# Optimization experiments

Measured on AMD Instinct MI355X. Metric: run time of the kernel, lower is better.

## Reference

```python
import jax, jax.numpy as jnp
import numpy as np

N_PRED = 29
F_DIM = 8192
H1 = 256
H2 = 128


def setup_inputs() -> dict:
    key = jax.random.key(0)
    ks = jax.random.split(key, 7)
    features = jax.random.normal(ks[0], (4096, F_DIM), dtype=jnp.float32)
    # Stacked per-predicate MLP weights (PyTorch Linear init scale ~ 1/sqrt(fan_in))
    W1 = jax.random.normal(ks[1], (N_PRED, F_DIM, H1), dtype=jnp.float32) / np.sqrt(F_DIM)
    b1 = jax.random.normal(ks[2], (N_PRED, H1), dtype=jnp.float32) / np.sqrt(F_DIM)
    W2 = jax.random.normal(ks[3], (N_PRED, H1, H2), dtype=jnp.float32) / np.sqrt(H1)
    b2 = jax.random.normal(ks[4], (N_PRED, H2), dtype=jnp.float32) / np.sqrt(H1)
    W3 = jax.random.normal(ks[5], (N_PRED, H2), dtype=jnp.float32) / np.sqrt(H2)
    b3 = jax.random.normal(ks[6], (N_PRED,), dtype=jnp.float32) / np.sqrt(H2)
    return {"features": features, "W1": W1, "b1": b1, "W2": W2, "b2": b2, "W3": W3, "b3": b3}


def reference(features, W1, b1, W2, b2, W3, b3):
    # 29 parallel heads as one batched (grouped) GEMM chain; dropout = identity (eval).
    h1 = jax.nn.relu(jnp.einsum('bf,pfh->bph', features, W1) + b1[None])   # [B, P, H1]
    h2 = jax.nn.relu(jnp.einsum('bph,phk->bpk', h1, W2) + b2[None])        # [B, P, H2]
    logits = jnp.einsum('bpk,pk->bp', h2, W3) + b3[None]                   # [B, P]
    return jax.nn.sigmoid(logits)
```

## Files before the change

### kernel.cpp

```cpp
#include <hip/hip_runtime.h>
#include <hip/hip_bf16.h>

typedef __attribute__((ext_vector_type(8))) short short8_t;
typedef __attribute__((ext_vector_type(8))) __bf16 bf16x8;
typedef __attribute__((ext_vector_type(4))) float f32x4;

__device__ __forceinline__ void gload16(const void* g, void* l) {
  __builtin_amdgcn_global_load_lds(
      (const __attribute__((address_space(1))) void*)g,
      (__attribute__((address_space(3))) void*)l, 16, 0, 0);
}

__device__ __forceinline__ unsigned short f2bf(float f) {
  __hip_bfloat16 h = __float2bfloat16(f);
  return __builtin_bit_cast(unsigned short, h);
}

#define BARRIER() asm volatile("s_barrier" ::: "memory")


__global__ void k_cvt_feat(const float* __restrict__ in, unsigned short* __restrict__ out) {
  const size_t N = (size_t)4096 * 8192;
  size_t i = ((size_t)blockIdx.x * 256 + threadIdx.x) * 4;
  const size_t stride = (size_t)gridDim.x * 256 * 4;
  for (; i < N; i += stride) {
    float4 v = *(const float4*)(in + i);
    ushort4 o;
    o.x = f2bf(v.x); o.y = f2bf(v.y); o.z = f2bf(v.z); o.w = f2bf(v.w);
    *(ushort4*)(out + i) = o;
  }
}

__global__ void k_cvt_w1(const float* __restrict__ W1, unsigned short* __restrict__ out, int p0) {
  __shared__ unsigned short t[64][262];
  const int p = p0 + blockIdx.z;
  const float* src = W1 + (size_t)p * 8192 * 256;
  unsigned short* dst = out + (size_t)blockIdx.z * 256 * 8192;
  const int f0 = blockIdx.x * 256, h0 = blockIdx.y * 64;
#pragma unroll
  for (int i = 0; i < 64; ++i) {
    int tt = i * 256 + threadIdx.x;
    int f = tt >> 6, c = tt & 63;
    t[c][f] = f2bf(src[(size_t)(f0 + f) * 256 + h0 + c]);
  }
  __syncthreads();
#pragma unroll
  for (int i = 0; i < 8; ++i) {
    int tt = i * 256 + threadIdx.x;
    int r = tt >> 5;
    int c8 = (tt & 31) * 8;
    short8_t o;
#pragma unroll
    for (int j = 0; j < 8; ++j) o[j] = (short)t[r][c8 + j];
    *(short8_t*)&dst[(size_t)(h0 + r) * 8192 + f0 + c8] = o;
  }
}

__global__ void k_cvt_w2(const float* __restrict__ W2, unsigned short* __restrict__ out) {
  const int p = blockIdx.x;
  const float* src = W2 + (size_t)p * 256 * 128;
  unsigned short* dst = out + (size_t)p * 128 * 256;
  for (int tt = threadIdx.x; tt < 128 * 256; tt += 256) {
    int j = tt >> 8, h = tt & 255;
    dst[tt] = f2bf(src[(size_t)h * 128 + j]);
  }
}

__global__ __launch_bounds__(512, 2) void k_gemm1(
    const unsigned short* __restrict__ A,
    const unsigned short* __restrict__ Bt,
    const float* __restrict__ b1,
    const unsigned short* __restrict__ W2t,
    const float* __restrict__ b2,
    const float* __restrict__ W3,
    const float* __restrict__ b3,
    float* __restrict__ out,
    int p0) {
  __shared__ __align__(16) unsigned short S[65536];

  const int tid = threadIdx.x;
  const int lane = tid & 63;
  const int wave = tid >> 6;
  const int sr = (wave >> 2) * 64;
  const int sc = (wave & 3) * 32;

  const int nwg = gridDim.x * gridDim.y;
  const int orig = blockIdx.y * gridDim.x + blockIdx.x;
  const int q = nwg >> 3, r_ = nwg & 7;
  const int xcd = orig & 7, idx = orig >> 3;
  const int wg = (xcd < r_ ? xcd * (q + 1) : r_ * (q + 1) + (xcd - r_) * q) + idx;
  const int mx = wg & 15;
  const int z = wg >> 4;
  const int p = p0 + z;
  const int m0 = mx * 256;

  const unsigned short* Ab = A + (size_t)m0 * 8192;
  const unsigned short* Bb = Bt + (size_t)z * 256 * 8192;

  int e0 = tid, r0 = e0 >> 3, u0 = (e0 & 7) ^ (r0 & 7);
  int e1 = 512 + tid, r1e = e1 >> 3, u1 = (e1 & 7) ^ (r1e & 7);
  const size_t s0 = (size_t)r0 * 8192 + u0 * 8;
  const size_t s1 = (size_t)r1e * 8192 + u1 * 8;
  const int ld0 = (wave * 64) * 8;
  const int ld1 = (512 + wave * 64) * 8;

  auto stage = [&](int buf, int isB, int h, int T) {
    const unsigned short* gb = (isB ? Bb : Ab) + (size_t)h * 128 * 8192 + (size_t)T * 64;
    unsigned short* lb = S + buf * 32768 + isB * 16384 + h * 8192;
    gload16(gb + s0, lb + ld0);
    gload16(gb + s1, lb + ld1);
  };

  const int l15 = lane & 15, ks = lane >> 4;

  auto rdA = [&](int buf, int h, int mi, int x) {
    int R = sr + mi * 16 + l15;
    int pu = (x * 4 + ks) ^ (R & 7);
    return __builtin_bit_cast(bf16x8, *(const short8_t*)(S + buf * 32768 + h * 8192 + R * 64 + pu * 8));
  };
  auto rdB = [&](int buf, int v, int nj, int x) {
    int R = sc + nj * 16 + l15;
    int pu = (x * 4 + ks) ^ (R & 7);
    return __builtin_bit_cast(bf16x8, *(const short8_t*)(S + buf * 32768 + 16384 + v * 8192 + R * 64 + pu * 8));
  };

  f32x4 acc[4][4][2] = {};
  const int NT = 8192 / 64;

  auto kstep = [&](int t, int pfa, int pf, int vm) {
    const int c = t & 1, nx = c ^ 1;
    bf16x8 a[4][2], bl[2][2], bh[2][2];
#pragma unroll
    for (int mi = 0; mi < 4; ++mi) { a[mi][0] = rdA(c, 0, mi, 0); a[mi][1] = rdA(c, 0, mi, 1); }
#pragma unroll
    for (int nj = 0; nj < 2; ++nj) { bl[nj][0] = rdB(c, 0, nj, 0); bl[nj][1] = rdB(c, 0, nj, 1); }
    if (pfa) stage(nx, 0, 1, t + 1);
    BARRIER();
    __builtin_amdgcn_s_setprio(1);
#pragma unroll
    for (int mi = 0; mi < 4; ++mi)
#pragma unroll
      for (int nj = 0; nj < 2; ++nj) {
        acc[0][mi][nj] = __builtin_amdgcn_mfma_f32_16x16x32_bf16(a[mi][0], bl[nj][0], acc[0][mi][nj], 0, 0, 0);
        acc[0][mi][nj] = __builtin_amdgcn_mfma_f32_16x16x32_bf16(a[mi][1], bl[nj][1], acc[0][mi][nj], 0, 0, 0);
      }
    __builtin_amdgcn_s_setprio(0);
    BARRIER();
#pragma unroll
    for (int nj = 0; nj < 2; ++nj) { bh[nj][0] = rdB(c, 1, nj, 0); bh[nj][1] = rdB(c, 1, nj, 1); }
    if (pf) stage(c, 0, 0, t + 2);
    BARRIER();
    __builtin_amdgcn_s_setprio(1);
#pragma unroll
    for (int mi = 0; mi < 4; ++mi)
#pragma unroll
      for (int nj = 0; nj < 2; ++nj) {
        acc[1][mi][nj] = __builtin_amdgcn_mfma_f32_16x16x32_bf16(a[mi][0], bh[nj][0], acc[1][mi][nj], 0, 0, 0);
        acc[1][mi][nj] = __builtin_amdgcn_mfma_f32_16x16x32_bf16(a[mi][1], bh[nj][1], acc[1][mi][nj], 0, 0, 0);
      }
    __builtin_amdgcn_s_setprio(0);
    BARRIER();
#pragma unroll
    for (int mi = 0; mi < 4; ++mi) { a[mi][0] = rdA(c, 1, mi, 0); a[mi][1] = rdA(c, 1, mi, 1); }
    if (pf) stage(c, 1, 1, t + 2);
    BARRIER();
    __builtin_amdgcn_s_setprio(1);
#pragma unroll
    for (int mi = 0; mi < 4; ++mi)
#pragma unroll
      for (int nj = 0; nj < 2; ++nj) {
        acc[2][mi][nj] = __builtin_amdgcn_mfma_f32_16x16x32_bf16(a[mi][0], bl[nj][0], acc[2][mi][nj], 0, 0, 0);
        acc[2][mi][nj] = __builtin_amdgcn_mfma_f32_16x16x32_bf16(a[mi][1], bl[nj][1], acc[2][mi][nj], 0, 0, 0);
      }
    __builtin_amdgcn_s_setprio(0);
    BARRIER();
    if (pf) stage(c, 1, 0, t + 2);
    __builtin_amdgcn_s_setprio(1);
#pragma unroll
    for (int mi = 0; mi < 4; ++mi)
#pragma unroll
      for (int nj = 0; nj < 2; ++nj) {
        acc[3][mi][nj] = __builtin_amdgcn_mfma_f32_16x16x32_bf16(a[mi][0], bh[nj][0], acc[3][mi][nj], 0, 0, 0);
        acc[3][mi][nj] = __builtin_amdgcn_mfma_f32_16x16x32_bf16(a[mi][1], bh[nj][1], acc[3][mi][nj], 0, 0, 0);
      }
    __builtin_amdgcn_s_setprio(0);
    if (vm == 6)      asm volatile("s_waitcnt vmcnt(6)" ::: "memory");
    else if (vm == 0) asm volatile("s_waitcnt vmcnt(0)" ::: "memory");
    BARRIER();
  };

  stage(0, 0, 0, 0); stage(0, 1, 0, 0); stage(0, 1, 1, 0); stage(0, 0, 1, 0);
  stage(1, 0, 0, 1); stage(1, 1, 1, 1); stage(1, 1, 0, 1);
  asm volatile("s_waitcnt vmcnt(6)" ::: "memory");
  BARRIER();

  for (int t = 0; t < NT - 2; ++t) kstep(t, 1, 1, 6);
  kstep(NT - 2, 1, 0, 0);
  kstep(NT - 1, 0, 0, -1);

  __syncthreads();
  {
    const int rg = lane >> 4;
#pragma unroll
    for (int qh = 0; qh < 2; ++qh)
#pragma unroll
      for (int qv = 0; qv < 2; ++qv) {
        const int qq = qh * 2 + qv;
#pragma unroll
        for (int nj = 0; nj < 2; ++nj) {
          const int c = qv * 128 + sc + nj * 16 + l15;
          const float bb = b1[p * 256 + c];
          const int u = c >> 3, sub = c & 7;
#pragma unroll
          for (int mi = 0; mi < 4; ++mi) {
            const int Rb = qh * 128 + sr + mi * 16 + rg * 4;
#pragma unroll
            for (int rr = 0; rr < 4; ++rr) {
              const int R = Rb + rr;
              float v = acc[qq][mi][nj][rr] + bb;
              v = v > 0.f ? v : 0.f;
              S[R * 256 + ((u ^ (R & 7)) * 8) + sub] = f2bf(v);
            }
          }
        }
      }
  }
  __syncthreads();
  {
    const unsigned short* Wp = W2t + (size_t)p * 128 * 256;
    f32x4 acc2[2][8] = {};
    bf16x8 bcur[8], bnxt[8];
#pragma unroll
    for (int nj = 0; nj < 8; ++nj)
      bcur[nj] = __builtin_bit_cast(bf16x8, *(const short8_t*)(Wp + (nj * 16 + l15) * 256 + ks * 8));
#pragma unroll
    for (int kt = 0; kt < 8; ++kt) {
      if (kt < 7) {
#pragma unroll
        for (int nj = 0; nj < 8; ++nj)
          bnxt[nj] = __builtin_bit_cast(bf16x8, *(const short8_t*)(Wp + (nj * 16 + l15) * 256 + (kt + 1) * 32 + ks * 8));
      }
      bf16x8 a2[2];
#pragma unroll
      for (int mi = 0; mi < 2; ++mi) {
        const int R = wave * 32 + mi * 16 + l15;
        const int u = kt * 4 + ks;
        a2[mi] = __builtin_bit_cast(bf16x8, *(const short8_t*)(S + R * 256 + ((u ^ (R & 7)) * 8)));
      }
#pragma unroll
      for (int mi = 0; mi < 2; ++mi)
#pragma unroll
        for (int nj = 0; nj < 8; ++nj)
          acc2[mi][nj] = __builtin_amdgcn_mfma_f32_16x16x32_bf16(a2[mi], bcur[nj], acc2[mi][nj], 0, 0, 0);
#pragma unroll
      for (int nj = 0; nj < 8; ++nj) bcur[nj] = bnxt[nj];
    }
    float b2v[8], w3v[8];
#pragma unroll
    for (int nj = 0; nj < 8; ++nj) {
      int c = nj * 16 + l15;
      b2v[nj] = b2[p * 128 + c];
      w3v[nj] = W3[p * 128 + c];
    }
    const float b3p = b3[p];
#pragma unroll
    for (int mi = 0; mi < 2; ++mi) {
#pragma unroll
      for (int r = 0; r < 4; ++r) {
        float s = 0.f;
#pragma unroll
        for (int nj = 0; nj < 8; ++nj) {
          float v = acc2[mi][nj][r] + b2v[nj];
          v = v > 0.f ? v : 0.f;
          s += v * w3v[nj];
        }
        s += __shfl_xor(s, 1);
        s += __shfl_xor(s, 2);
        s += __shfl_xor(s, 4);
        s += __shfl_xor(s, 8);
        if (l15 == 0) {
          int m = m0 + wave * 32 + mi * 16 + ks * 4 + r;
          float logit = s + b3p;
          out[(size_t)m * 29 + p] = 1.f / (1.f + __expf(-logit));
        }
      }
    }
  }
}

extern "C" void kernel_launch(void* const* d_in, const int* in_sizes, int n_in,
                              void* d_out, int out_size, void* d_ws, size_t ws_size,
                              hipStream_t stream) {
  const float* features = (const float*)d_in[0];
  const float* W1 = (const float*)d_in[1];
  const float* b1 = (const float*)d_in[2];
  const float* W2 = (const float*)d_in[3];
  const float* b2 = (const float*)d_in[4];
  const float* W3 = (const float*)d_in[5];
  const float* b3 = (const float*)d_in[6];
  float* out = (float*)d_out;

  char* ws = (char*)d_ws;
  const size_t featB = (size_t)4096 * 8192 * 2;
  const size_t w2B   = (size_t)29 * 128 * 256 * 2;
  const size_t w1pp  = (size_t)256 * 8192 * 2;

  unsigned short* featbf = (unsigned short*)ws;
  unsigned short* w2t    = (unsigned short*)(ws + featB);
  unsigned short* w1t    = (unsigned short*)(ws + featB + w2B);

  size_t base = featB + w2B;
  size_t rem = (ws_size > base) ? (ws_size - base) : 0;
  int CH = (int)(rem / w1pp);
  if (CH > 29) CH = 29;
  if (CH < 1) CH = 1;

  k_cvt_feat<<<2048, 256, 0, stream>>>(features, featbf);
  k_cvt_w2<<<29, 256, 0, stream>>>(W2, w2t);

  for (int p0 = 0; p0 < 29; p0 += CH) {
    int c = (29 - p0) < CH ? (29 - p0) : CH;
    k_cvt_w1<<<dim3(32, 4, c), 256, 0, stream>>>(W1, w1t, p0);
    k_gemm1<<<dim3(16, c), 512, 0, stream>>>(featbf, w1t, b1, w2t, b2, W3, b3, out, p0);
  }
}
```

Measured before the change: 547.0 us.

## Software-pipeline LDS fragment reads across k-steps and reduce barriers

Restructures the GEMM main loop so the next tile's A-low and B-low fragments are read from LDS at the end of the current k-step, overlapping with the final MFMA block. Fragments are kept as persistent register arrays across iterations, and several barriers per k-step are removed. The aim is to hide LDS read latency behind MFMA work. The cost is higher register pressure, which may lower occupancy, and a more delicate ordering between LDS writes and reads.

Result: faster. 531.8 us, median of 4 (-2.8%).

```diff
diff --git a/kernel.cpp b/kernel.cpp
--- a/kernel.cpp
+++ b/kernel.cpp
@@ -125,78 +125,82 @@
   };
 
   f32x4 acc[4][4][2] = {};
+  bf16x8 aH0[4][2], aH1[4][2], blf[2][2], bhf[2][2];
   const int NT = 8192 / 64;
 
-  auto kstep = [&](int t, int pfa, int pf, int vm) {
+  auto kstep = [&](int t, int pfa, int pf, int ra, int vm) {
     const int c = t & 1, nx = c ^ 1;
-    bf16x8 a[4][2], bl[2][2], bh[2][2];
-#pragma unroll
-    for (int mi = 0; mi < 4; ++mi) { a[mi][0] = rdA(c, 0, mi, 0); a[mi][1] = rdA(c, 0, mi, 1); }
-#pragma unroll
-    for (int nj = 0; nj < 2; ++nj) { bl[nj][0] = rdB(c, 0, nj, 0); bl[nj][1] = rdB(c, 0, nj, 1); }
+    BARRIER();
+#pragma unroll
+    for (int nj = 0; nj < 2; ++nj) { bhf[nj][0] = rdB(c, 1, nj, 0); bhf[nj][1] = rdB(c, 1, nj, 1); }
     if (pfa) stage(nx, 0, 1, t + 1);
-    BARRIER();
     __builtin_amdgcn_s_setprio(1);
 #pragma unroll
     for (int mi = 0; mi < 4; ++mi)
 #pragma unroll
       for (int nj = 0; nj < 2; ++nj) {
-        acc[0][mi][nj] = __builtin_amdgcn_mfma_f32_16x16x32_bf16(a[mi][0], bl[nj][0], acc[0][mi][nj], 0, 0, 0);
-        acc[0][mi][nj] = __builtin_amdgcn_mfma_f32_16x16x32_bf16(a[mi][1], bl[nj][1], acc[0][mi][nj], 0, 0, 0);
+        acc[0][mi][nj] = __builtin_amdgcn_mfma_f32_16x16x32_bf16(aH0[mi][0], blf[nj][0], acc[0][mi][nj], 0, 0, 0);
+        acc[0][mi][nj] = __builtin_amdgcn_mfma_f32_16x16x32_bf16(aH0[mi][1], blf[nj][1], acc[0][mi][nj], 0, 0, 0);
       }
     __builtin_amdgcn_s_setprio(0);
     BARRIER();
 #pragma unroll
-    for (int nj = 0; nj < 2; ++nj) { bh[nj][0] = rdB(c, 1, nj, 0); bh[nj][1] = rdB(c, 1, nj, 1); }
+    for (int mi = 0; mi < 4; ++mi) { aH1[mi][0] = rdA(c, 1, mi, 0); aH1[mi][1] = rdA(c, 1, mi, 1); }
     if (pf) stage(c, 0, 0, t + 2);
-    BARRIER();
     __builtin_amdgcn_s_setprio(1);
 #pragma unroll
     for (int mi = 0; mi < 4; ++mi)
 #pragma unroll
       for (int nj = 0; nj < 2; ++nj) {
-        acc[1][mi][nj] = __builtin_amdgcn_mfma_f32_16x16x32_bf16(a[mi][0], bh[nj][0], acc[1][mi][nj], 0, 0, 0);
-        acc[1][mi][nj] = __builtin_amdgcn_mfma_f32_16x16x32_bf16(a[mi][1], bh[nj][1], acc[1][mi][nj], 0, 0, 0);
+        acc[1][mi][nj] = __builtin_amdgcn_mfma_f32_16x16x32_bf16(aH0[mi][0], bhf[nj][0], acc[1][mi][nj], 0, 0, 0);
+        acc[1][mi][nj] = __builtin_amdgcn_mfma_f32_16x16x32_bf16(aH0[mi][1], bhf[nj][1], acc[1][mi][nj], 0, 0, 0);
       }
     __builtin_amdgcn_s_setprio(0);
     BARRIER();
-#pragma unroll
-    for (int mi = 0; mi < 4; ++mi) { a[mi][0] = rdA(c, 1, mi, 0); a[mi][1] = rdA(c, 1, mi, 1); }
     if (pf) stage(c, 1, 1, t + 2);
-    BARRIER();
     __builtin_amdgcn_s_setprio(1);
 #pragma unroll
     for (int mi = 0; mi < 4; ++mi)
 #pragma unroll
       for (int nj = 0; nj < 2; ++nj) {
-        acc[2][mi][nj] = __builtin_amdgcn_mfma_f32_16x16x32_bf16(a[mi][0], bl[nj][0], acc[2][mi][nj], 0, 0, 0);
-        acc[2][mi][nj] = __builtin_amdgcn_mfma_f32_16x16x32_bf16(a[mi][1], bl[nj][1], acc[2][mi][nj], 0, 0, 0);
+        acc[2][mi][nj] = __builtin_amdgcn_mfma_f32_16x16x32_bf16(aH1[mi][0], blf[nj][0], acc[2][mi][nj], 0, 0, 0);
+        acc[2][mi][nj] = __builtin_amdgcn_mfma_f32_16x16x32_bf16(aH1[mi][1], blf[nj][1], acc[2][mi][nj], 0, 0, 0);
       }
     __builtin_amdgcn_s_setprio(0);
     BARRIER();
     if (pf) stage(c, 1, 0, t + 2);
-    __builtin_amdgcn_s_setprio(1);
-#pragma unroll
-    for (int mi = 0; mi < 4; ++mi)
-#pragma unroll
-      for (int nj = 0; nj < 2; ++nj) {
-        acc[3][mi][nj] = __builtin_amdgcn_mfma_f32_16x16x32_bf16(a[mi][0], bh[nj][0], acc[3][mi][nj], 0, 0, 0);
-        acc[3][mi][nj] = __builtin_amdgcn_mfma_f32_16x16x32_bf16(a[mi][1], bh[nj][1], acc[3][mi][nj], 0, 0, 0);
-      }
-    __builtin_amdgcn_s_setprio(0);
     if (vm == 6)      asm volatile("s_waitcnt vmcnt(6)" ::: "memory");
     else if (vm == 0) asm volatile("s_waitcnt vmcnt(0)" ::: "memory");
     BARRIER();
+    if (ra) {
+#pragma unroll
+      for (int mi = 0; mi < 4; ++mi) { aH0[mi][0] = rdA(nx, 0, mi, 0); aH0[mi][1] = rdA(nx, 0, mi, 1); }
+#pragma unroll
+      for (int nj = 0; nj < 2; ++nj) { blf[nj][0] = rdB(nx, 0, nj, 0); blf[nj][1] = rdB(nx, 0, nj, 1); }
+    }
+    __builtin_amdgcn_s_setprio(1);
+#pragma unroll
+    for (int mi = 0; mi < 4; ++mi)
+#pragma unroll
+      for (int nj = 0; nj < 2; ++nj) {
+        acc[3][mi][nj] = __builtin_amdgcn_mfma_f32_16x16x32_bf16(aH1[mi][0], bhf[nj][0], acc[3][mi][nj], 0, 0, 0);
+        acc[3][mi][nj] = __builtin_amdgcn_mfma_f32_16x16x32_bf16(aH1[mi][1], bhf[nj][1], acc[3][mi][nj], 0, 0, 0);
+      }
+    __builtin_amdgcn_s_setprio(0);
   };
 
   stage(0, 0, 0, 0); stage(0, 1, 0, 0); stage(0, 1, 1, 0); stage(0, 0, 1, 0);
   stage(1, 0, 0, 1); stage(1, 1, 1, 1); stage(1, 1, 0, 1);
   asm volatile("s_waitcnt vmcnt(6)" ::: "memory");
   BARRIER();
-
-  for (int t = 0; t < NT - 2; ++t) kstep(t, 1, 1, 6);
-  kstep(NT - 2, 1, 0, 0);
-  kstep(NT - 1, 0, 0, -1);
+#pragma unroll
+  for (int mi = 0; mi < 4; ++mi) { aH0[mi][0] = rdA(0, 0, mi, 0); aH0[mi][1] = rdA(0, 0, mi, 1); }
+#pragma unroll
+  for (int nj = 0; nj < 2; ++nj) { blf[nj][0] = rdB(0, 0, nj, 0); blf[nj][1] = rdB(0, 0, nj, 1); }
+
+  for (int t = 0; t < NT - 2; ++t) kstep(t, 1, 1, 1, 6);
+  kstep(NT - 2, 1, 0, 1, 0);
+  kstep(NT - 1, 0, 0, 0, -1);
 
   __syncthreads();
   {
```

## Load A fragments directly from global into registers; triple-buffer B in LDS

Applied to the files above, without the earlier changes.

The first GEMM's main loop is restructured. Each wave now owns a 64x128 output tile (4x2 wave grid) instead of 64x32 sub-quadrants. Only the W1 (B) operand is staged through LDS, with a 3-deep ring buffer and one barrier per k-step. The feature (A) fragments are loaded straight from global memory into registers and double-buffered across k-steps. This cuts LDS traffic and barrier count, but A now uses uncoalesced per-lane 16-byte global loads and A reuse across waves depends on the cache.

After: 776.9 us. 1.42x slower.

```diff
diff --git a/kernel.cpp b/kernel.cpp
--- a/kernel.cpp
+++ b/kernel.cpp
@@ -81,8 +81,8 @@
   const int tid = threadIdx.x;
   const int lane = tid & 63;
   const int wave = tid >> 6;
-  const int sr = (wave >> 2) * 64;
-  const int sc = (wave & 3) * 32;
+  const int wm = wave >> 1;
+  const int wn = wave & 1;
 
   const int nwg = gridDim.x * gridDim.y;
   const int orig = blockIdx.y * gridDim.x + blockIdx.x;
@@ -97,133 +97,106 @@
   const unsigned short* Ab = A + (size_t)m0 * 8192;
   const unsigned short* Bb = Bt + (size_t)z * 256 * 8192;
 
-  int e0 = tid, r0 = e0 >> 3, u0 = (e0 & 7) ^ (r0 & 7);
-  int e1 = 512 + tid, r1e = e1 >> 3, u1 = (e1 & 7) ^ (r1e & 7);
-  const size_t s0 = (size_t)r0 * 8192 + u0 * 8;
-  const size_t s1 = (size_t)r1e * 8192 + u1 * 8;
-  const int ld0 = (wave * 64) * 8;
-  const int ld1 = (512 + wave * 64) * 8;
-
-  auto stage = [&](int buf, int isB, int h, int T) {
-    const unsigned short* gb = (isB ? Bb : Ab) + (size_t)h * 128 * 8192 + (size_t)T * 64;
-    unsigned short* lb = S + buf * 32768 + isB * 16384 + h * 8192;
-    gload16(gb + s0, lb + ld0);
-    gload16(gb + s1, lb + ld1);
-  };
-
   const int l15 = lane & 15, ks = lane >> 4;
 
-  auto rdA = [&](int buf, int h, int mi, int x) {
-    int R = sr + mi * 16 + l15;
+  const unsigned short* aLane = Ab + (size_t)(wm * 64 + l15) * 8192 + ks * 8;
+
+  unsigned sOff[4];
+  int ldOff[4];
+#pragma unroll
+  for (int i = 0; i < 4; ++i) {
+    int e = wave * 256 + i * 64 + lane;
+    int r = e >> 3, u = (e & 7) ^ (r & 7);
+    sOff[i] = r * 8192 + u * 8;
+    ldOff[i] = e * 8;
+  }
+  auto stageB = [&](int buf, int T) {
+    unsigned short* lb = S + buf * 16384;
+    const unsigned short* gb = Bb + (size_t)T * 64;
+#pragma unroll
+    for (int i = 0; i < 4; ++i) gload16(gb + sOff[i], lb + ldOff[i]);
+  };
+
+  auto rdB = [&](int buf, int nj, int x) {
+    int R = wn * 128 + nj * 16 + l15;
     int pu = (x * 4 + ks) ^ (R & 7);
-    return __builtin_bit_cast(bf16x8, *(const short8_t*)(S + buf * 32768 + h * 8192 + R * 64 + pu * 8));
-  };
-  auto rdB = [&](int buf, int v, int nj, int x) {
-    int R = sc + nj * 16 + l15;
-    int pu = (x * 4 + ks) ^ (R & 7);
-    return __builtin_bit_cast(bf16x8, *(const short8_t*)(S + buf * 32768 + 16384 + v * 8192 + R * 64 + pu * 8));
-  };
-
-  f32x4 acc[4][4][2] = {};
-  const int NT = 8192 / 64;
-
-  auto kstep = [&](int t, int pfa, int pf, int vm) {
-    const int c = t & 1, nx = c ^ 1;
-    bf16x8 a[4][2], bl[2][2], bh[2][2];
-#pragma unroll
-    for (int mi = 0; mi < 4; ++mi) { a[mi][0] = rdA(c, 0, mi, 0); a[mi][1] = rdA(c, 0, mi, 1); }
-#pragma unroll
-    for (int nj = 0; nj < 2; ++nj) { bl[nj][0] = rdB(c, 0, nj, 0); bl[nj][1] = rdB(c, 0, nj, 1); }
-    if (pfa) stage(nx, 0, 1, t + 1);
-    BARRIER();
+    return __builtin_bit_cast(bf16x8, *(const short8_t*)(S + buf * 16384 + R * 64 + pu * 8));
+  };
+
+  auto loadA = [&](bf16x8 (&a)[4][2], int T) {
+#pragma unroll
+    for (int mi = 0; mi < 4; ++mi)
+#pragma unroll
+      for (int x = 0; x < 2; ++x)
+        a[mi][x] = __builtin_bit_cast(bf16x8,
+            *(const short8_t*)(aLane + (size_t)mi * 131072 + (size_t)T * 64 + x * 32));
+  };
+
+  f32x4 acc[4][8] = {};
+  bf16x8 aA[4][2], aB[4][2];
+  const int NT = 128;
+
+  auto kstep = [&](int t, bf16x8 (&aC)[4][2], bf16x8 (&aN)[4][2]) {
+    const int cur = t % 3;
+    if (t + 2 < NT) stageB((t + 2) % 3, t + 2);
+    bf16x8 b[4][2];
+#pragma unroll
+    for (int nj = 0; nj < 4; ++nj) { b[nj][0] = rdB(cur, nj, 0); b[nj][1] = rdB(cur, nj, 1); }
+    if (t + 2 < NT) asm volatile("s_waitcnt vmcnt(4)" ::: "memory");
+    else            asm volatile("s_waitcnt vmcnt(0)" ::: "memory");
     __builtin_amdgcn_s_setprio(1);
 #pragma unroll
     for (int mi = 0; mi < 4; ++mi)
 #pragma unroll
-      for (int nj = 0; nj < 2; ++nj) {
-        acc[0][mi][nj] = __builtin_amdgcn_mfma_f32_16x16x32_bf16(a[mi][0], bl[nj][0], acc[0][mi][nj], 0, 0, 0);
-        acc[0][mi][nj] = __builtin_amdgcn_mfma_f32_16x16x32_bf16(a[mi][1], bl[nj][1], acc[0][mi][nj], 0, 0, 0);
+      for (int nj = 0; nj < 4; ++nj) {
+        acc[mi][nj] = __builtin_amdgcn_mfma_f32_16x16x32_bf16(aC[mi][0], b[nj][0], acc[mi][nj], 0, 0, 0);
+        acc[mi][nj] = __builtin_amdgcn_mfma_f32_16x16x32_bf16(aC[mi][1], b[nj][1], acc[mi][nj], 0, 0, 0);
+      }
+    __builtin_amdgcn_s_setprio(0);
+#pragma unroll
+    for (int nj = 0; nj < 4; ++nj) { b[nj][0] = rdB(cur, nj + 4, 0); b[nj][1] = rdB(cur, nj + 4, 1); }
+    if (t + 1 < NT) loadA(aN, t + 1);
+    __builtin_amdgcn_s_setprio(1);
+#pragma unroll
+    for (int mi = 0; mi < 4; ++mi)
+#pragma unroll
+      for (int nj = 0; nj < 4; ++nj) {
+        acc[mi][nj + 4] = __builtin_amdgcn_mfma_f32_16x16x32_bf16(aC[mi][0], b[nj][0], acc[mi][nj + 4], 0, 0, 0);
+        acc[mi][nj + 4] = __builtin_amdgcn_mfma_f32_16x16x32_bf16(aC[mi][1], b[nj][1], acc[mi][nj + 4], 0, 0, 0);
       }
     __builtin_amdgcn_s_setprio(0);
     BARRIER();
-#pragma unroll
-    for (int nj = 0; nj < 2; ++nj) { bh[nj][0] = rdB(c, 1, nj, 0); bh[nj][1] = rdB(c, 1, nj, 1); }
-    if (pf) stage(c, 0, 0, t + 2);
-    BARRIER();
-    __builtin_amdgcn_s_setprio(1);
-#pragma unroll
-    for (int mi = 0; mi < 4; ++mi)
-#pragma unroll
-      for (int nj = 0; nj < 2; ++nj) {
-        acc[1][mi][nj] = __builtin_amdgcn_mfma_f32_16x16x32_bf16(a[mi][0], bh[nj][0], acc[1][mi][nj], 0, 0, 0);
-        acc[1][mi][nj] = __builtin_amdgcn_mfma_f32_16x16x32_bf16(a[mi][1], bh[nj][1], acc[1][mi][nj], 0, 0, 0);
-      }
-    __builtin_amdgcn_s_setprio(0);
-    BARRIER();
-#pragma unroll
-    for (int mi = 0; mi < 4; ++mi) { a[mi][0] = rdA(c, 1, mi, 0); a[mi][1] = rdA(c, 1, mi, 1); }
-    if (pf) stage(c, 1, 1, t + 2);
-    BARRIER();
-    __builtin_amdgcn_s_setprio(1);
-#pragma unroll
-    for (int mi = 0; mi < 4; ++mi)
-#pragma unroll
-      for (int nj = 0; nj < 2; ++nj) {
-        acc[2][mi][nj] = __builtin_amdgcn_mfma_f32_16x16x32_bf16(a[mi][0], bl[nj][0], acc[2][mi][nj], 0, 0, 0);
-        acc[2][mi][nj] = __builtin_amdgcn_mfma_f32_16x16x32_bf16(a[mi][1], bl[nj][1], acc[2][mi][nj], 0, 0, 0);
-      }
-    __builtin_amdgcn_s_setprio(0);
-    BARRIER();
-    if (pf) stage(c, 1, 0, t + 2);
-    __builtin_amdgcn_s_setprio(1);
-#pragma unroll
-    for (int mi = 0; mi < 4; ++mi)
-#pragma unroll
-      for (int nj = 0; nj < 2; ++nj) {
-        acc[3][mi][nj] = __builtin_amdgcn_mfma_f32_16x16x32_bf16(a[mi][0], bh[nj][0], acc[3][mi][nj], 0, 0, 0);
-        acc[3][mi][nj] = __builtin_amdgcn_mfma_f32_16x16x32_bf16(a[mi][1], bh[nj][1], acc[3][mi][nj], 0, 0, 0);
-      }
-    __builtin_amdgcn_s_setprio(0);
-    if (vm == 6)      asm volatile("s_waitcnt vmcnt(6)" ::: "memory");
-    else if (vm == 0) asm volatile("s_waitcnt vmcnt(0)" ::: "memory");
-    BARRIER();
-  };
-
-  stage(0, 0, 0, 0); stage(0, 1, 0, 0); stage(0, 1, 1, 0); stage(0, 0, 1, 0);
-  stage(1, 0, 0, 1); stage(1, 1, 1, 1); stage(1, 1, 0, 1);
-  asm volatile("s_waitcnt vmcnt(6)" ::: "memory");
+  };
+
+  stageB(0, 0); stageB(1, 1);
+  loadA(aA, 0);
+  asm volatile("s_waitcnt vmcnt(12)" ::: "memory");
   BARRIER();
 
-  for (int t = 0; t < NT - 2; ++t) kstep(t, 1, 1, 6);
-  kstep(NT - 2, 1, 0, 0);
-  kstep(NT - 1, 0, 0, -1);
+  for (int t = 0; t < NT; t += 2) {
+    kstep(t, aA, aB);
+    kstep(t + 1, aB, aA);
+  }
 
   __syncthreads();
   {
-    const int rg = lane >> 4;
-#pragma unroll
-    for (int qh = 0; qh < 2; ++qh)
-#pragma unroll
-      for (int qv = 0; qv < 2; ++qv) {
-        const int qq = qh * 2 + qv;
-#pragma unroll
-        for (int nj = 0; nj < 2; ++nj) {
-          const int c = qv * 128 + sc + nj * 16 + l15;
-          const float bb = b1[p * 256 + c];
-          const int u = c >> 3, sub = c & 7;
-#pragma unroll
-          for (int mi = 0; mi < 4; ++mi) {
-            const int Rb = qh * 128 + sr + mi * 16 + rg * 4;
-#pragma unroll
-            for (int rr = 0; rr < 4; ++rr) {
-              const int R = Rb + rr;
-              float v = acc[qq][mi][nj][rr] + bb;
-              v = v > 0.f ? v : 0.f;
-              S[R * 256 + ((u ^ (R & 7)) * 8) + sub] = f2bf(v);
-            }
-          }
+#pragma unroll
+    for (int nj = 0; nj < 8; ++nj) {
+      const int c = wn * 128 + nj * 16 + l15;
+      const float bb = b1[p * 256 + c];
+      const int u = c >> 3, sub = c & 7;
+#pragma unroll
+      for (int mi = 0; mi < 4; ++mi) {
+        const int Rb = wm * 64 + mi * 16 + ks * 4;
+#pragma unroll
+        for (int rr = 0; rr < 4; ++rr) {
+          const int R = Rb + rr;
+          float v = acc[mi][nj][rr] + bb;
+          v = v > 0.f ? v : 0.f;
+          S[R * 256 + ((u ^ (R & 7)) * 8) + sub] = f2bf(v);
         }
       }
+    }
   }
   __syncthreads();
   {
```
